# Performance work log

Hardware: AMD Instinct MI355X
Metric: run time of the kernel (lower is better)

Reference implementation:

```python
import jax, jax.numpy as jnp
import numpy as np

# geomloss SamplesLoss('sinkhorn', p=1, blur=0.01, reach=None, debias=True)
P = 1
EPS = 0.01  # temperature = blur**p
N_ITERS = 32
LOSS_WEIGHT = 1.0


def setup_inputs() -> dict:
    key = jax.random.key(0)
    kx, ky = jax.random.split(key)
    x = jax.random.normal(kx, (6144, 3), dtype=jnp.float32)
    y = jax.random.normal(ky, (6144, 3), dtype=jnp.float32)
    return {"x": x, "y": y}


def _cost(x, y):
    # p=1 cost: Euclidean distance ||x_i - y_j||, via expanded quadratic form
    x2 = jnp.sum(x * x, axis=-1)  # [N]
    y2 = jnp.sum(y * y, axis=-1)  # [M]
    d2 = x2[:, None] + y2[None, :] - 2.0 * (x @ y.T)  # [N, M]
    return jnp.sqrt(jnp.maximum(d2, 0.0) + 1e-12)


def _softmin(C, h):
    # h: [M] = log_weights + dual/eps ; returns [N] = -eps*LSE_j(h_j - C_ij/eps)
    return -EPS * jax.scipy.special.logsumexp(h[None, :] - C / EPS, axis=1)


def _sinkhorn_potentials(C_xy, loga, logb):
    # symmetric log-domain Sinkhorn with averaged updates (geomloss style)
    N, M = C_xy.shape
    f0 = jnp.zeros((N,), C_xy.dtype)
    g0 = jnp.zeros((M,), C_xy.dtype)

    def step(carry, _):
        f, g = carry
        ft = _softmin(C_xy, logb + g / EPS)
        gt = _softmin(C_xy.T, loga + f / EPS)
        return (0.5 * (f + ft), 0.5 * (g + gt)), None

    (f, g), _ = jax.lax.scan(step, (f0, g0), None, length=N_ITERS)
    # final non-averaged extrapolation step
    f_fin = _softmin(C_xy, logb + g / EPS)
    g_fin = _softmin(C_xy.T, loga + f / EPS)
    return f_fin, g_fin


def _sym_potential(C_xx, logw):
    # debias term: symmetric fixed point p = softmin(C_xx, logw + p/eps)
    N = C_xx.shape[0]

    def step(p, _):
        return 0.5 * (p + _softmin(C_xx, logw + p / EPS)), None

    p, _ = jax.lax.scan(step, jnp.zeros((N,), C_xx.dtype), None, length=N_ITERS)
    return _softmin(C_xx, logw + p / EPS)


def reference(x, y):
    N, M = x.shape[0], y.shape[0]
    a = jnp.full((N,), 1.0 / N, x.dtype)
    b = jnp.full((M,), 1.0 / M, y.dtype)
    loga = jnp.log(a)
    logb = jnp.log(b)

    C_xy = _cost(x, y)
    C_xx = _cost(x, x)
    C_yy = _cost(y, y)

    f, g = _sinkhorn_potentials(C_xy, loga, logb)
    p_x = _sym_potential(C_xx, loga)
    p_y = _sym_potential(C_yy, logb)

    # debiased Sinkhorn divergence: <a, f - p_x> + <b, g - p_y>
    loss = jnp.sum(a * (f - p_x)) + jnp.sum(b * (g - p_y))
    return LOSS_WEIGHT * loss
```

## Files before the change

### kernel.cpp

```cpp
#include <hip/hip_runtime.h>
#include <math.h>

#ifndef __has_builtin
#define __has_builtin(x) 0
#endif

__device__ __forceinline__ float fexp2(float x) {
#if __has_builtin(__builtin_amdgcn_exp2f)
  return __builtin_amdgcn_exp2f(x);
#else
  return exp2f(x);
#endif
}
__device__ __forceinline__ float flog2(float x) {
#if __has_builtin(__builtin_amdgcn_logf)
  return __builtin_amdgcn_logf(x);
#else
  return log2f(x);
#endif
}
__device__ __forceinline__ float fsqrt_(float x) {
#if __has_builtin(__builtin_amdgcn_sqrtf)
  return __builtin_amdgcn_sqrtf(x);
#else
  return sqrtf(x);
#endif
}

constexpr int   NP    = 6144;
constexpr float LOG2E = 1.44269504088896340736f;
constexpr float EPS_F = 0.01f;
constexpr float KKc   = LOG2E / EPS_F;
constexpr float NKKc  = -KKc;
constexpr float LBc   = -8.72323127482750f;
constexpr float HBc   = LBc * LOG2E;
constexpr float NEL2c = -EPS_F * 0.693147180559945f;

constexpr int RPW  = 8;
constexpr int RPB  = 32;
constexpr int NRB  = NP / RPB;
constexpr int NTL  = NP / 64;
constexpr int CELLS = 4096;

__device__ __forceinline__ unsigned cell_of(float v) {
  int c = (int)floorf((v + 4.0f) * 2.0f);
  return (unsigned)min(15, max(0, c));
}
__device__ __forceinline__ unsigned morton12(unsigned cx, unsigned cy, unsigned cz) {
  unsigned m = 0;
#pragma unroll
  for (int b = 0; b < 4; ++b)
    m |= (((cx >> b) & 1u) << (3 * b)) | (((cy >> b) & 1u) << (3 * b + 1)) |
         (((cz >> b) & 1u) << (3 * b + 2));
  return m;
}

__global__ __launch_bounds__(1024) void sort_kernel(
    const float* __restrict__ xin, const float* __restrict__ yin,
    float4* __restrict__ Xp, float4* __restrict__ Xq,
    float4* __restrict__ Yp, float4* __restrict__ Yq,
    float4* __restrict__ XaLo, float4* __restrict__ XaHi,
    float4* __restrict__ YaLo, float4* __restrict__ YaHi,
    float* __restrict__ stA, float* __restrict__ hmaxA)
{
  __shared__ unsigned hist[CELLS];
  __shared__ unsigned offs[CELLS];
  __shared__ unsigned wsum[64];
  const int tid = threadIdx.x;
  const float* src = (blockIdx.x == 0) ? xin : yin;
  float4* Pp  = (blockIdx.x == 0) ? Xp : Yp;
  float4* Pq  = (blockIdx.x == 0) ? Xq : Yq;
  float4* aLo = (blockIdx.x == 0) ? XaLo : YaLo;
  float4* aHi = (blockIdx.x == 0) ? XaHi : YaHi;

  for (int i = tid; i < CELLS; i += 1024) { hist[i] = 0u; offs[i] = 0u; }
  for (int i = tid; i < 2 * NP; i += 1024) stA[blockIdx.x * 2 * NP + i] = 0.f;
  for (int i = tid; i < 2 * NRB; i += 1024) hmaxA[blockIdx.x * 2 * NRB + i] = 0.f;
  __syncthreads();

  for (int i = tid; i < NP; i += 1024) {
    float a0 = src[3*i], a1 = src[3*i+1], a2 = src[3*i+2];
    unsigned m = morton12(cell_of(a0), cell_of(a1), cell_of(a2));
    atomicAdd(&hist[m], 1u);
  }
  __syncthreads();
  if (tid < 64) {
    unsigned s = 0;
    for (int j = 0; j < 64; ++j) { unsigned v = hist[tid*64+j]; hist[tid*64+j] = s; s += v; }
    wsum[tid] = s;
  }
  __syncthreads();
  if (tid == 0) {
    unsigned s = 0;
    for (int j = 0; j < 64; ++j) { unsigned v = wsum[j]; wsum[j] = s; s += v; }
  }
  __syncthreads();
  if (tid < 64) {
    unsigned o = wsum[tid];
    for (int j = 0; j < 64; ++j) hist[tid*64+j] += o;
  }
  __syncthreads();
  for (int i = tid; i < NP; i += 1024) {
    float a0 = src[3*i], a1 = src[3*i+1], a2 = src[3*i+2];
    unsigned m = morton12(cell_of(a0), cell_of(a1), cell_of(a2));
    unsigned dst = hist[m] + atomicAdd(&offs[m], 1u);
    float an = fmaf(a0, a0, fmaf(a1, a1, a2 * a2));
    Pp[dst] = make_float4(a0, a1, a2, an);
    Pq[dst] = make_float4(-2.f*a0, -2.f*a1, -2.f*a2, an);
  }
  __syncthreads();
  const int wave = tid >> 6, lane = tid & 63;
  for (int t = wave; t < NTL; t += 16) {
    float4 p = Pp[t * 64 + lane];
    float lx = p.x, ly = p.y, lz = p.z, hx = p.x, hy = p.y, hz = p.z;
#pragma unroll
    for (int off = 32; off; off >>= 1) {
      lx = fminf(lx, __shfl_xor(lx, off)); hx = fmaxf(hx, __shfl_xor(hx, off));
      ly = fminf(ly, __shfl_xor(ly, off)); hy = fmaxf(hy, __shfl_xor(hy, off));
      lz = fminf(lz, __shfl_xor(lz, off)); hz = fmaxf(hz, __shfl_xor(hz, off));
    }
    if (lane == 0) {
      aLo[t] = make_float4(lx, ly, lz, 0.f);
      aHi[t] = make_float4(hx, hy, hz, 0.f);
    }
  }
}

__global__ __launch_bounds__(256, 4) void softmin_pass(
    const float4* __restrict__ Xp, const float4* __restrict__ Yp,
    const float4* __restrict__ Xq, const float4* __restrict__ Yq,
    const float4* __restrict__ XaLo, const float4* __restrict__ XaHi,
    const float4* __restrict__ YaLo, const float4* __restrict__ YaHi,
    const float* __restrict__ stIn, const float* __restrict__ hmaxIn,
    float* __restrict__ stOut, float* __restrict__ hmaxOut, int avg)
{
  const int bid  = blockIdx.x;
  const int sub  = bid & 3;
  const int rb   = bid >> 2;
  const int tid  = threadIdx.x;
  const int lane = tid & 63;
  const int wave = tid >> 6;
  const int wrow0 = rb * RPB + wave * RPW;

  const float4 *P4, *Q4, *aLo, *aHi;
  const float *hsrc, *hpair, *oldp; float* outp;
  if (sub == 0) {
    P4 = Xp; Q4 = Yq; aLo = YaLo; aHi = YaHi;
    hsrc = stIn + NP;     hpair = hmaxIn + NRB;     oldp = stIn;          outp = stOut;
  } else if (sub == 1) {
    P4 = Yp; Q4 = Xq; aLo = XaLo; aHi = XaHi;
    hsrc = stIn;          hpair = hmaxIn;           oldp = stIn + NP;     outp = stOut + NP;
  } else if (sub == 2) {
    P4 = Xp; Q4 = Xq; aLo = XaLo; aHi = XaHi;
    hsrc = stIn + 2*NP;   hpair = hmaxIn + 2*NRB;   oldp = stIn + 2*NP;   outp = stOut + 2*NP;
  } else {
    P4 = Yp; Q4 = Yq; aLo = YaLo; aHi = YaHi;
    hsrc = stIn + 3*NP;   hpair = hmaxIn + 3*NRB;   oldp = stIn + 3*NP;   outp = stOut + 3*NP;
  }

  float pxr[RPW], pyr[RPW], pzr[RPW], pwr[RPW], mr[RPW], sr[RPW], m40r[RPW];
  float rlx, rly, rlz, rhx, rhy, rhz;
#pragma unroll
  for (int r = 0; r < RPW; ++r) {
    float4 p = P4[wrow0 + r];
    pxr[r] = p.x; pyr[r] = p.y; pzr[r] = p.z; pwr[r] = p.w;
    if (r == 0) { rlx = rhx = p.x; rly = rhy = p.y; rlz = rhz = p.z; }
    else {
      rlx = fminf(rlx, p.x); rhx = fmaxf(rhx, p.x);
      rly = fminf(rly, p.y); rhy = fmaxf(rhy, p.y);
      rlz = fminf(rlz, p.z); rhz = fmaxf(rhz, p.z);
    }
  }

  float b0, b1, uc0, uc1;
  {
    auto tile_bounds = [&](int t, float& b, float& uc) {
      float4 lo = aLo[t], hi = aHi[t];
      float gx = fmaxf(fmaxf(lo.x - rhx, rlx - hi.x), 0.f);
      float gy = fmaxf(fmaxf(lo.y - rhy, rly - hi.y), 0.f);
      float gz = fmaxf(fmaxf(lo.z - rhz, rlz - hi.z), 0.f);
      float dmin = fsqrt_(fmaf(gx, gx, fmaf(gy, gy, gz * gz)));
      float fx = fmaxf(hi.x - rlx, rhx - lo.x);
      float fy = fmaxf(hi.y - rly, rhy - lo.y);
      float fz = fmaxf(hi.z - rlz, rhz - lo.z);
      float dmax = fsqrt_(fmaf(fx, fx, fmaf(fy, fy, fz * fz)));
      float hraw = fmaxf(hpair[2 * t], hpair[2 * t + 1]);
      float hh = fmaf(KKc, hraw, HBc);
      b  = fmaf(NKKc, dmin, hh);
      uc = fmaf(NKKc, dmax, hh);
    };
    tile_bounds(lane, b0, uc0);
    int tB = (lane < 32) ? (64 + lane) : 95;
    tile_bounds(tB, b1, uc1);
    if (lane >= 32) { b1 = -INFINITY; uc1 = -INFINITY; }
  }
  float ulb = fmaxf(uc0, uc1);
#pragma unroll
  for (int off = 32; off; off >>= 1) ulb = fmaxf(ulb, __shfl_xor(ulb, off));
  const float thr = ulb - 40.f;
  unsigned long long mA = __ballot(b0 >= thr);
  unsigned long long mB = __ballot(b1 >= thr);

#pragma unroll
  for (int r = 0; r < RPW; ++r) { mr[r] = ulb; sr[r] = 0.f; m40r[r] = ulb + 40.f; }

  auto proc = [&](int t) {
    int j = t * 64 + lane;
    float4 q = Q4[j];
    float hh = fmaf(KKc, hsrc[j], HBc);
#pragma unroll
    for (int r = 0; r < RPW; ++r) {
      float dot = fmaf(pxr[r], q.x, fmaf(pyr[r], q.y, fmaf(pzr[r], q.z, q.w)));
      float d2  = pwr[r] + dot;
      float c   = fsqrt_(fmaxf(d2, 1e-12f));
      float u   = fmaf(NKKc, c, hh);
      if (__any(u > m40r[r])) {
        float mn = fmaxf(mr[r], u);
        sr[r] *= fexp2(mr[r] - mn);
        mr[r] = mn; m40r[r] = mn + 40.f;
      }
      sr[r] += fexp2(u - mr[r]);
    }
  };
  while (mA) { int t = __ffsll(mA) - 1;  mA &= mA - 1; proc(t); }
  while (mB) { int t = 63 + __ffsll(mB); mB &= mB - 1; proc(t); }

  __shared__ float wmaxLds[4];
  float wmax = -INFINITY;
#pragma unroll
  for (int r = 0; r < RPW; ++r) {
    float m = mr[r], s = sr[r];
#pragma unroll
    for (int off = 32; off; off >>= 1) {
      float mo = __shfl_xor(m, off);
      float so = __shfl_xor(s, off);
      float mn = fmaxf(m, mo);
      s = s * fexp2(m - mn) + so * fexp2(mo - mn);
      m = mn;
    }
    float val = NEL2c * (m + flog2(s));
    const int row = wrow0 + r;
    float wv = avg ? 0.5f * (oldp[row] + val) : val;
    if (lane == 0) outp[row] = wv;
    wmax = fmaxf(wmax, wv);
  }
  if (lane == 0) wmaxLds[wave] = wmax;
  __syncthreads();
  if (tid == 0)
    hmaxOut[sub * NRB + rb] =
        fmaxf(fmaxf(wmaxLds[0], wmaxLds[1]), fmaxf(wmaxLds[2], wmaxLds[3]));
}

__global__ __launch_bounds__(256) void loss_kernel(
    const float* __restrict__ st, float* __restrict__ out)
{
  double acc = 0.0;
  for (int i = threadIdx.x; i < NP; i += 256)
    acc += (double)(st[i] - st[i + 2*NP]) + (double)(st[i + NP] - st[i + 3*NP]);
  __shared__ double red[4];
#pragma unroll
  for (int off = 32; off; off >>= 1) acc += __shfl_xor(acc, off);
  const int lane = threadIdx.x & 63, wave = threadIdx.x >> 6;
  if (lane == 0) red[wave] = acc;
  __syncthreads();
  if (threadIdx.x == 0)
    out[0] = (float)((red[0] + red[1] + red[2] + red[3]) * (1.0 / NP));
}

extern "C" void kernel_launch(void* const* d_in, const int* in_sizes, int n_in,
                              void* d_out, int out_size, void* d_ws, size_t ws_size,
                              hipStream_t stream)
{
  const float* x = (const float*)d_in[0];
  const float* y = (const float*)d_in[1];
  float* out = (float*)d_out;
  float* ws  = (float*)d_ws;

  float4* Xp = (float4*)ws;
  float4* Xq = (float4*)(ws + 4 * NP);
  float4* Yp = (float4*)(ws + 8 * NP);
  float4* Yq = (float4*)(ws + 12 * NP);
  float*  p  = ws + 16 * NP;
  float4* XaLo = (float4*)p; p += 4 * NTL;
  float4* XaHi = (float4*)p; p += 4 * NTL;
  float4* YaLo = (float4*)p; p += 4 * NTL;
  float4* YaHi = (float4*)p; p += 4 * NTL;
  float* stA = p;            p += 4 * NP;
  float* stB = p;            p += 4 * NP;
  float* hmA = p;            p += 4 * NRB;
  float* hmB = p;

  hipLaunchKernelGGL(sort_kernel, dim3(2), dim3(1024), 0, stream,
                     x, y, Xp, Xq, Yp, Yq, XaLo, XaHi, YaLo, YaHi, stA, hmA);

  float* cur = stA; float* nxt = stB;
  float* hmCur = hmA; float* hmNxt = hmB;
  for (int it = 0; it <= 32; ++it) {
    const int avg = (it < 32) ? 1 : 0;
    hipLaunchKernelGGL(softmin_pass, dim3(4 * NRB), dim3(256), 0, stream,
                       Xp, Yp, Xq, Yq, XaLo, XaHi, YaLo, YaHi,
                       cur, hmCur, nxt, hmNxt, avg);
    float* t = cur; cur = nxt; nxt = t;
    t = hmCur; hmCur = hmNxt; hmNxt = t;
  }

  hipLaunchKernelGGL(loss_kernel, dim3(1), dim3(256), 0, stream, cur, out);
}
```

Before: 2.385 ms.

## Add per-point bounding-sphere culling with LDS compaction ring for softmin columns

```diff
diff --git a/kernel.cpp b/kernel.cpp
--- a/kernel.cpp
+++ b/kernel.cpp
@@ -35,6 +35,7 @@
 constexpr float LBc   = -8.72323127482750f;
 constexpr float HBc   = LBc * LOG2E;
 constexpr float NEL2c = -EPS_F * 0.693147180559945f;
+constexpr float WIN   = 40.f;
 
 constexpr int RPW  = 8;
 constexpr int RPB  = 32;
@@ -134,6 +135,10 @@
     const float* __restrict__ stIn, const float* __restrict__ hmaxIn,
     float* __restrict__ stOut, float* __restrict__ hmaxOut, int avg)
 {
+  __shared__ float4 ringQ[4][256];
+  __shared__ float  ringH[4][256];
+  __shared__ float  wmaxLds[4];
+
   const int bid  = blockIdx.x;
   const int sub  = bid & 3;
   const int rb   = bid >> 2;
@@ -171,6 +176,15 @@
       rlz = fminf(rlz, p.z); rhz = fmaxf(rhz, p.z);
     }
   }
+  const float cx = 0.5f * (rlx + rhx), cy = 0.5f * (rly + rhy), cz = 0.5f * (rlz + rhz);
+  const float cw = fmaf(cx, cx, fmaf(cy, cy, cz * cz));
+  float rrad = 0.f;
+#pragma unroll
+  for (int r = 0; r < RPW; ++r) {
+    float dx = pxr[r] - cx, dy = pyr[r] - cy, dz = pzr[r] - cz;
+    rrad = fmaxf(rrad, fmaf(dx, dx, fmaf(dy, dy, dz * dz)));
+  }
+  rrad = fsqrt_(rrad);
 
   float b0, b1, uc0, uc1;
   {
@@ -197,17 +211,35 @@
   float ulb = fmaxf(uc0, uc1);
 #pragma unroll
   for (int off = 32; off; off >>= 1) ulb = fmaxf(ulb, __shfl_xor(ulb, off));
-  const float thr = ulb - 40.f;
+  const float thr0 = ulb - WIN;
+  unsigned long long m0A = __ballot(b0 >= thr0);
+  unsigned long long m0B = __ballot(b1 >= thr0);
+
+  float ulbl = -INFINITY;
+  {
+    auto refine = [&](int t) {
+      int j = t * 64 + lane;
+      float4 q = Q4[j];
+      float hh = fmaf(KKc, hsrc[j], HBc);
+      float d2c = q.w + fmaf(q.x, cx, fmaf(q.y, cy, fmaf(q.z, cz, cw)));
+      float d = fsqrt_(fmaxf(d2c, 0.f));
+      ulbl = fmaxf(ulbl, fmaf(NKKc, d + rrad, hh));
+    };
+    unsigned long long a = m0A, b = m0B;
+    while (a) { int t = __ffsll(a) - 1;  a &= a - 1; refine(t); }
+    while (b) { int t = 63 + __ffsll(b); b &= b - 1; refine(t); }
+  }
+#pragma unroll
+  for (int off = 32; off; off >>= 1) ulbl = fmaxf(ulbl, __shfl_xor(ulbl, off));
+  ulb = fmaxf(ulb, ulbl);
+  const float thr = ulb - WIN;
   unsigned long long mA = __ballot(b0 >= thr);
   unsigned long long mB = __ballot(b1 >= thr);
 
 #pragma unroll
-  for (int r = 0; r < RPW; ++r) { mr[r] = ulb; sr[r] = 0.f; m40r[r] = ulb + 40.f; }
-
-  auto proc = [&](int t) {
-    int j = t * 64 + lane;
-    float4 q = Q4[j];
-    float hh = fmaf(KKc, hsrc[j], HBc);
+  for (int r = 0; r < RPW; ++r) { mr[r] = ulb; sr[r] = 0.f; m40r[r] = ulb + WIN; }
+
+  auto inner8 = [&](float4 q, float hh) {
 #pragma unroll
     for (int r = 0; r < RPW; ++r) {
       float dot = fmaf(pxr[r], q.x, fmaf(pyr[r], q.y, fmaf(pzr[r], q.z, q.w)));
@@ -217,15 +249,54 @@
       if (__any(u > m40r[r])) {
         float mn = fmaxf(mr[r], u);
         sr[r] *= fexp2(mr[r] - mn);
-        mr[r] = mn; m40r[r] = mn + 40.f;
+        mr[r] = mn; m40r[r] = mn + WIN;
       }
       sr[r] += fexp2(u - mr[r]);
     }
   };
-  while (mA) { int t = __ffsll(mA) - 1;  mA &= mA - 1; proc(t); }
-  while (mB) { int t = 63 + __ffsll(mB); mB &= mB - 1; proc(t); }
-
-  __shared__ float wmaxLds[4];
+
+  int headq = 0, tailq = 0;
+  {
+    auto testchunk = [&](int t) {
+      int j = t * 64 + lane;
+      float4 q = Q4[j];
+      float hh = fmaf(KKc, hsrc[j], HBc);
+      float d2c = q.w + fmaf(q.x, cx, fmaf(q.y, cy, fmaf(q.z, cz, cw)));
+      float d = fsqrt_(fmaxf(d2c, 0.f));
+      float uhi = fmaf(NKKc, fmaxf(d - rrad, 0.f), hh);
+      bool keep = (uhi >= thr);
+      unsigned long long k = __ballot(keep);
+      if (k) {
+        int my = __builtin_amdgcn_mbcnt_hi((unsigned)(k >> 32),
+                 __builtin_amdgcn_mbcnt_lo((unsigned)k, 0u));
+        if (keep) {
+          int slot = (tailq + my) & 255;
+          ringQ[wave][slot] = q;
+          ringH[wave][slot] = hh;
+        }
+        tailq += (int)__popcll(k);
+        while (tailq - headq >= 64) {
+          int slot = (headq + lane) & 255;
+          float4 qq = ringQ[wave][slot];
+          float  hq = ringH[wave][slot];
+          headq += 64;
+          inner8(qq, hq);
+        }
+      }
+    };
+    unsigned long long a = mA, b = mB;
+    while (a) { int t = __ffsll(a) - 1;  a &= a - 1; testchunk(t); }
+    while (b) { int t = 63 + __ffsll(b); b &= b - 1; testchunk(t); }
+    int rem = tailq - headq;
+    if (rem > 0) {
+      int slot = (headq + lane) & 255;
+      float4 qq = ringQ[wave][slot];
+      float  hq = ringH[wave][slot];
+      if (lane >= rem) { qq = make_float4(0.f, 0.f, 0.f, 0.f); hq = -INFINITY; }
+      inner8(qq, hq);
+    }
+  }
+
   float wmax = -INFINITY;
 #pragma unroll
   for (int r = 0; r < RPW; ++r) {
```

After: 2.984 ms. 25.1% more time.
